# Optimization experiments

Measured on AMD Instinct MI355X. Metric: run time of the kernel, lower is better.

The kernel has to match this reference:

```python
import jax, jax.numpy as jnp
import numpy as np

HEADS = 16
PHI = (1.0 + np.sqrt(5.0)) / 2.0


def setup_inputs() -> dict:
    key = jax.random.key(0)
    k1, k2, k3, k4 = jax.random.split(key, 4)
    B, L, D = 2, 2048, 1024
    x = jax.random.normal(k1, (B, L, D), dtype=jnp.float32)
    # nn.Linear(dim, 3*dim, bias=False): store as [D, 3D] for x @ W
    w_qkv = jax.random.normal(k2, (D, 3 * D), dtype=jnp.float32) * (D ** -0.5)
    w_proj = jax.random.normal(k3, (D, D), dtype=jnp.float32) * (D ** -0.5)
    b_proj = jax.random.normal(k4, (D,), dtype=jnp.float32) * 0.01
    return {"x": x, "w_qkv": w_qkv, "w_proj": w_proj, "b_proj": b_proj}


def phi_bias(L):
    # pos[i] = (i * phi) mod 1 ; bias = log(exp(-|pos_i - pos_j|) + 1e-8)
    pos = (jnp.arange(L, dtype=jnp.float32) * PHI) % 1.0
    dist = jnp.abs(pos[:, None] - pos[None, :])  # [L, L]
    return jnp.log(jnp.exp(-dist) + 1e-8)


def reference(x, w_qkv, w_proj, b_proj):
    B, L, D = x.shape
    H = HEADS
    Dh = D // H
    scale = Dh ** -0.5
    qkv = (x @ w_qkv).reshape(B, L, 3, H, Dh)
    q = jnp.transpose(qkv[:, :, 0], (0, 2, 1, 3))  # [B, H, L, Dh]
    k = jnp.transpose(qkv[:, :, 1], (0, 2, 1, 3))
    v = jnp.transpose(qkv[:, :, 2], (0, 2, 1, 3))
    attn = jnp.einsum("bhid,bhjd->bhij", q, k) * scale  # [B, H, L, L]
    attn = attn + phi_bias(L)[None, None]  # additive phi-distance bias
    attn = jax.nn.softmax(attn, axis=-1)
    out = jnp.einsum("bhij,bhjd->bhid", attn, v)  # [B, H, L, Dh]
    out = jnp.transpose(out, (0, 2, 1, 3)).reshape(B, L, D)
    return out @ w_proj + b_proj
```

## Files before the change

### kernel.cpp

```cpp
#include <hip/hip_runtime.h>
#include <math.h>


typedef _Float16 f16;
typedef _Float16 f16x4 __attribute__((ext_vector_type(4)));
typedef _Float16 f16x8 __attribute__((ext_vector_type(8)));
typedef float f32x4 __attribute__((ext_vector_type(4)));

#define MFMA32(a, b, c) __builtin_amdgcn_mfma_f32_16x16x32_f16(a, b, c, 0, 0, 0)

static constexpr int Bsz = 2, Lseq = 2048, Dm = 1024, H = 16, Dh = 64;
static constexpr int Mtot = Bsz * Lseq;
static constexpr int NQKV = 3 * Dm;
static constexpr float PHI_F = 1.61803398874989484820f;
static constexpr float LOG2E = 1.44269504088896f;
static constexpr float QS = 0.125f * LOG2E;
static constexpr float CSTEP = 0.55417527999932633f;

__device__ __forceinline__ void load16_to_lds(const f16* g, f16* l) {
  __builtin_amdgcn_global_load_lds(
      (const __attribute__((address_space(1))) unsigned int*)g,
      (__attribute__((address_space(3))) unsigned int*)l, 16, 0, 0);
}

__global__ __launch_bounds__(256) void cast_f32_f16(const float* __restrict__ in,
                                                    f16* __restrict__ out, int n) {
  int i = (blockIdx.x * 256 + threadIdx.x) * 4;
  if (i < n) {
    float4 v = *reinterpret_cast<const float4*>(in + i);
    f16 t[4] = {(f16)v.x, (f16)v.y, (f16)v.z, (f16)v.w};
    *reinterpret_cast<uint2*>(out + i) = *reinterpret_cast<uint2*>(t);
  }
}

__global__ __launch_bounds__(256) void transpose_cast(const float* __restrict__ in,
                                                      f16* __restrict__ out,
                                                      int K, int N) {
  __shared__ float tile[32][33];
  int n0 = blockIdx.x * 32, k0 = blockIdx.y * 32;
  int tx = threadIdx.x & 31, ty = threadIdx.x >> 5;
#pragma unroll
  for (int r = 0; r < 32; r += 8)
    tile[ty + r][tx] = in[(size_t)(k0 + ty + r) * N + n0 + tx];
  __syncthreads();
#pragma unroll
  for (int r = 0; r < 32; r += 8)
    out[(size_t)(n0 + ty + r) * K + k0 + tx] = (f16)tile[tx][ty + r];
}

__global__ __launch_bounds__(256) void v_transpose(const f16* __restrict__ in,
                                                   f16* __restrict__ out) {
  __shared__ f16 td[64][68];
  int bh = blockIdx.y, l0 = blockIdx.x * 64;
  int tid = threadIdx.x;
  const f16* src = in + (size_t)bh * Lseq * Dh;
#pragma unroll
  for (int c = tid; c < 512; c += 256) {
    int row = c >> 3, col = (c & 7) * 8;
    uint4 v = *reinterpret_cast<const uint4*>(src + (size_t)(l0 + row) * Dh + col);
    f16 tmp[8];
    *reinterpret_cast<uint4*>(tmp) = v;
#pragma unroll
    for (int j = 0; j < 8; j++) td[col + j][row] = tmp[j];
  }
  __syncthreads();
  f16* dst = out + (size_t)bh * Dh * Lseq;
#pragma unroll
  for (int c = tid; c < 512; c += 256) {
    int d = c >> 3, m = (c & 7) * 8;
    f16 tmp[8];
#pragma unroll
    for (int j = 0; j < 8; j++) tmp[j] = td[d][m + j];
    *reinterpret_cast<uint4*>(dst + (size_t)d * Lseq + l0 + m) =
        *reinterpret_cast<uint4*>(tmp);
  }
}

template <int MODE>
__global__ __launch_bounds__(256) void gemm_f16(
    const f16* __restrict__ A, const f16* __restrict__ Bt,
    int M, int N, int K,
    f16* __restrict__ qb, f16* __restrict__ kb, f16* __restrict__ vl,
    float* __restrict__ out, const float* __restrict__ bias) {
  constexpr int BM = (MODE == 0) ? 128 : 64;
  constexpr int MI = BM / 32;
  constexpr int AI = BM / 32;
  __shared__ f16 As[BM * 64];
  __shared__ f16 Bs[128 * 64];

  int tid = threadIdx.x;
  int wave = tid >> 6, lane = tid & 63;
  int quad = lane >> 4, l16 = lane & 15;
  int wm = (wave >> 1) * (MI * 16), wn = (wave & 1) * 64;

  int lid = blockIdx.x;
  int xcd = lid & 7, t = lid >> 3;
  int m0, n0;
  if (MODE == 0) {
    int mg = xcd >> 1, ng = xcd & 1;
    m0 = (mg * 8 + t / 12) * 128;
    n0 = (ng * 12 + t % 12) * 128;
  } else {
    m0 = (xcd * 8 + (t >> 3)) * 64;
    n0 = (t & 7) * 128;
  }

  const int gu = (lane & 7) ^ ((lane >> 3) & 7);
  const f16* gA[AI];
  f16* lA[AI];
#pragma unroll
  for (int i = 0; i < AI; i++) {
    int it = wave * AI + i;
    gA[i] = A + (size_t)(m0 + it * 8 + (lane >> 3)) * K + gu * 8;
    lA[i] = As + it * 512;
  }
  const f16* gB[4];
  f16* lB[4];
#pragma unroll
  for (int i = 0; i < 4; i++) {
    int it = wave * 4 + i;
    gB[i] = Bt + (size_t)(n0 + it * 8 + (lane >> 3)) * K + gu * 8;
    lB[i] = Bs + it * 512;
  }

  f32x4 acc[MI][4] = {};

  for (int k0 = 0; k0 < K; k0 += 64) {
#pragma unroll
    for (int i = 0; i < AI; i++) load16_to_lds(gA[i] + k0, lA[i]);
#pragma unroll
    for (int i = 0; i < 4; i++) load16_to_lds(gB[i] + k0, lB[i]);
    __syncthreads();
#pragma unroll
    for (int s = 0; s < 2; s++) {
      f16x8 a[MI], b[4];
#pragma unroll
      for (int i = 0; i < MI; i++) {
        int row = wm + i * 16 + l16;
        a[i] = *reinterpret_cast<const f16x8*>(
            As + row * 64 + (((s * 4 + quad) ^ (l16 & 7)) * 8));
      }
#pragma unroll
      for (int j = 0; j < 4; j++) {
        int row = wn + j * 16 + l16;
        b[j] = *reinterpret_cast<const f16x8*>(
            Bs + row * 64 + (((s * 4 + quad) ^ (l16 & 7)) * 8));
      }
#pragma unroll
      for (int i = 0; i < MI; i++)
#pragma unroll
        for (int j = 0; j < 4; j++)
          acc[i][j] = MFMA32(a[i], b[j], acc[i][j]);
    }
    __syncthreads();
  }

#pragma unroll
  for (int i = 0; i < MI; i++) {
#pragma unroll
    for (int j = 0; j < 4; j++) {
      int n = n0 + wn + j * 16 + l16;
#pragma unroll
      for (int r = 0; r < 4; r++) {
        int m = m0 + wm + i * 16 + quad * 4 + r;
        if (MODE == 0) {
          int ty = n >> 10;
          int df = n & 1023;
          int h = df >> 6, dh = df & 63;
          int b = m >> 11, l = m & 2047;
          size_t idx = (((size_t)(b * H + h)) * Lseq + l) * Dh + dh;
          if (ty == 0)
            qb[idx] = (f16)(acc[i][j][r] * QS);
          else if (ty == 1)
            kb[idx] = (f16)acc[i][j][r];
          else
            vl[idx] = (f16)acc[i][j][r];
        } else {
          out[(size_t)m * N + n] = acc[i][j][r] + bias[n];
        }
      }
    }
  }
}

__global__ __launch_bounds__(256, 4) void attn_kernel(
    const f16* __restrict__ qb,
    const f16* __restrict__ kb,
    const f16* __restrict__ vb,
    f16* __restrict__ ctx) {
  __shared__ __align__(16) unsigned char smem[17408];
  f16* Ks = (f16*)smem;
  f16* Vs = (f16*)(smem + 9216);

  int bh = blockIdx.y;
  int q0 = blockIdx.x * 64;
  int tid = threadIdx.x, wave = tid >> 6, lane = tid & 63;
  int quad = lane >> 4, l16 = lane & 15;
  int jhalf = wave >> 1, qhalf = wave & 1;

  f16x8 qfrag[2][2];
  float pq[2];
#pragma unroll
  for (int set = 0; set < 2; set++) {
    int q = q0 + qhalf * 32 + set * 16 + l16;
    const f16* Qrow = qb + ((size_t)bh * Lseq + q) * Dh;
    qfrag[set][0] = *reinterpret_cast<const f16x8*>(Qrow + quad * 8);
    qfrag[set][1] = *reinterpret_cast<const f16x8*>(Qrow + 32 + quad * 8);
    pq[set] = fmodf((float)q * PHI_F, 1.0f);
  }

  float pk[2][4];
#pragma unroll
  for (int jb = 0; jb < 2; jb++)
#pragma unroll
    for (int r = 0; r < 4; r++) {
      int j = jhalf * 32 + jb * 16 + quad * 4 + r;
      pk[jb][r] = fmodf((float)j * PHI_F, 1.0f);
    }

  int uoff0 = ((jhalf * 4 + 0 + (quad >> 1)) ^ (l16 & 7)) * 8 + (quad & 1) * 4;
  int uoff1 = ((jhalf * 4 + 2 + (quad >> 1)) ^ (l16 & 7)) * 8 + (quad & 1) * 4;

  const f16 one = (f16)1.0f;
  const f16x8 ones8 = {one, one, one, one, one, one, one, one};

  f32x4 acc_o[2][4] = {};
  f32x4 acc_l[2] = {};

  const f16* Kbh = kb + (size_t)bh * Lseq * Dh;
  const f16* Vbh = vb + (size_t)bh * Dh * Lseq;

  for (int j0 = 0; j0 < Lseq; j0 += 64) {
    __syncthreads();
#pragma unroll
    for (int c = tid; c < 512; c += 256) {
      int row = c >> 3, col = (c & 7) * 8;
      *reinterpret_cast<uint4*>(Ks + row * 72 + col) =
          *reinterpret_cast<const uint4*>(Kbh + (size_t)(j0 + row) * Dh + col);
    }
#pragma unroll
    for (int c = tid; c < 512; c += 256) {
      int row = c >> 3, u = c & 7;
      int us = u ^ (row & 7);
      *reinterpret_cast<uint4*>(Vs + row * 64 + us * 8) =
          *reinterpret_cast<const uint4*>(Vbh + (size_t)row * Lseq + j0 + u * 8);
    }
    __syncthreads();

    f32x4 accs[2][2] = {};
#pragma unroll
    for (int s = 0; s < 2; s++)
#pragma unroll
      for (int jb = 0; jb < 2; jb++) {
        f16x8 kf = *reinterpret_cast<const f16x8*>(
            Ks + (jhalf * 32 + jb * 16 + l16) * 72 + s * 32 + quad * 8);
        accs[0][jb] = MFMA32(kf, qfrag[0][s], accs[0][jb]);
        accs[1][jb] = MFMA32(kf, qfrag[1][s], accs[1][jb]);
      }

    f16x8 pf8[2];
#pragma unroll
    for (int set = 0; set < 2; set++) {
#pragma unroll
      for (int jb = 0; jb < 2; jb++) {
        float p[4];
#pragma unroll
        for (int r = 0; r < 4; r++) {
          float d = pq[set] - pk[jb][r];
          float arg = fmaf(-LOG2E, fabsf(d), accs[set][jb][r]);
          p[r] = __builtin_amdgcn_exp2f(arg);
        }
        auto lo = __builtin_amdgcn_cvt_pkrtz(p[0], p[1]);
        auto hi = __builtin_amdgcn_cvt_pkrtz(p[2], p[3]);
        pf8[set][jb * 4 + 0] = lo[0];
        pf8[set][jb * 4 + 1] = lo[1];
        pf8[set][jb * 4 + 2] = hi[0];
        pf8[set][jb * 4 + 3] = hi[1];
      }
      acc_l[set] = MFMA32(ones8, pf8[set], acc_l[set]);
    }
#pragma unroll
    for (int jb = 0; jb < 2; jb++)
#pragma unroll
      for (int r = 0; r < 4; r++) {
        float tt = pk[jb][r] + CSTEP;
        pk[jb][r] = tt - floorf(tt);
      }

#pragma unroll
    for (int dblk = 0; dblk < 4; dblk++) {
      const f16* vrow = Vs + (dblk * 16 + l16) * 64;
      f16x4 v0 = *reinterpret_cast<const f16x4*>(vrow + uoff0);
      f16x4 v1 = *reinterpret_cast<const f16x4*>(vrow + uoff1);
      f16x8 va;
      va[0] = v0[0]; va[1] = v0[1]; va[2] = v0[2]; va[3] = v0[3];
      va[4] = v1[0]; va[5] = v1[1]; va[6] = v1[2]; va[7] = v1[3];
      acc_o[0][dblk] = MFMA32(va, pf8[0], acc_o[0][dblk]);
      acc_o[1][dblk] = MFMA32(va, pf8[1], acc_o[1][dblk]);
    }
  }

  __syncthreads();
  float* Oex = (float*)smem;
  float* Lex = (float*)(smem + 16384);
  if (jhalf == 1) {
#pragma unroll
    for (int set = 0; set < 2; set++) {
#pragma unroll
      for (int dblk = 0; dblk < 4; dblk++)
#pragma unroll
        for (int r = 0; r < 4; r++)
          Oex[(((qhalf * 2 + set) * 4 + dblk) * 16 + quad * 4 + r) * 16 + l16] =
              acc_o[set][dblk][r];
      if (quad == 0) Lex[(qhalf * 2 + set) * 16 + l16] = acc_l[set][0];
    }
  }
  __syncthreads();
  if (jhalf == 0) {
    int b = bh >> 4, h = bh & 15;
#pragma unroll
    for (int set = 0; set < 2; set++) {
      float ltot = acc_l[set][0] + Lex[(qhalf * 2 + set) * 16 + l16];
      float inv = 1.0f / ltot;
      int q = q0 + qhalf * 32 + set * 16 + l16;
      f16* crow = ctx + (size_t)(b * Lseq + q) * Dm + h * 64;
#pragma unroll
      for (int dblk = 0; dblk < 4; dblk++) {
        f16x4 o;
#pragma unroll
        for (int r = 0; r < 4; r++) {
          float full = acc_o[set][dblk][r] +
              Oex[(((qhalf * 2 + set) * 4 + dblk) * 16 + quad * 4 + r) * 16 + l16];
          o[r] = (f16)(full * inv);
        }
        *reinterpret_cast<uint2*>(crow + dblk * 16 + quad * 4) =
            *reinterpret_cast<uint2*>(&o);
      }
    }
  }
}

extern "C" void kernel_launch(void* const* d_in, const int* in_sizes, int n_in,
                              void* d_out, int out_size, void* d_ws, size_t ws_size,
                              hipStream_t stream) {
  const float* x      = (const float*)d_in[0];
  const float* w_qkv  = (const float*)d_in[1];
  const float* w_proj = (const float*)d_in[2];
  const float* b_proj = (const float*)d_in[3];
  float* out = (float*)d_out;

  f16* xb    = (f16*)d_ws;
  f16* wqkvT = xb + (size_t)Mtot * Dm;
  f16* wpT   = wqkvT + (size_t)NQKV * Dm;
  f16* qb    = wpT + (size_t)Dm * Dm;
  f16* kb    = qb + (size_t)Bsz * H * Lseq * Dh;
  f16* vb    = kb + (size_t)Bsz * H * Lseq * Dh;
  f16* ctx   = vb + (size_t)Bsz * H * Lseq * Dh;
  f16* vl    = ctx;

  cast_f32_f16<<<(Mtot * Dm) / (256 * 4), 256, 0, stream>>>(x, xb, Mtot * Dm);
  transpose_cast<<<dim3(NQKV / 32, Dm / 32), 256, 0, stream>>>(w_qkv, wqkvT, Dm, NQKV);
  transpose_cast<<<dim3(Dm / 32, Dm / 32), 256, 0, stream>>>(w_proj, wpT, Dm, Dm);

  gemm_f16<0><<<768, 256, 0, stream>>>(
      xb, wqkvT, Mtot, NQKV, Dm, qb, kb, vl, nullptr, nullptr);

  v_transpose<<<dim3(Lseq / 64, Bsz * H), 256, 0, stream>>>(vl, vb);

  attn_kernel<<<dim3(Lseq / 64, Bsz * H), 256, 0, stream>>>(qb, kb, vb, ctx);

  gemm_f16<1><<<512, 256, 0, stream>>>(
      ctx, wpT, Mtot, Dm, Dm, nullptr, nullptr, nullptr, out, b_proj);
}
```

Measured before the change: 205.0 us.

## Use direct global-to-LDS loads for K/V tiles and pre-permute V layout

Measured after the change: 192.5 us. -6.1%, faster.

```diff
diff --git a/kernel.cpp b/kernel.cpp
--- a/kernel.cpp
+++ b/kernel.cpp
@@ -67,11 +67,14 @@
   f16* dst = out + (size_t)bh * Dh * Lseq;
 #pragma unroll
   for (int c = tid; c < 512; c += 256) {
-    int d = c >> 3, m = (c & 7) * 8;
+    int d = c >> 3, co = c & 7;
+    int jh = co >> 2, qd = co & 3;
     f16 tmp[8];
 #pragma unroll
-    for (int j = 0; j < 8; j++) tmp[j] = td[d][m + j];
-    *reinterpret_cast<uint4*>(dst + (size_t)d * Lseq + l0 + m) =
+    for (int e = 0; e < 4; e++) tmp[e] = td[d][jh * 32 + qd * 4 + e];
+#pragma unroll
+    for (int e = 0; e < 4; e++) tmp[4 + e] = td[d][jh * 32 + 16 + qd * 4 + e];
+    *reinterpret_cast<uint4*>(dst + (size_t)d * Lseq + l0 + co * 8) =
         *reinterpret_cast<uint4*>(tmp);
   }
 }
@@ -105,7 +108,7 @@
     n0 = (t & 7) * 128;
   }
 
-  const int gu = (lane & 7) ^ ((lane >> 3) & 7);
+  const int gu = (lane & 7) ^ (lane >> 3);
   const f16* gA[AI];
   f16* lA[AI];
 #pragma unroll
@@ -188,9 +191,9 @@
     const f16* __restrict__ kb,
     const f16* __restrict__ vb,
     f16* __restrict__ ctx) {
-  __shared__ __align__(16) unsigned char smem[17408];
+  __shared__ __align__(16) unsigned char smem[16640];
   f16* Ks = (f16*)smem;
-  f16* Vs = (f16*)(smem + 9216);
+  f16* Vs = (f16*)(smem + 8192);
 
   int bh = blockIdx.y;
   int q0 = blockIdx.x * 64;
@@ -218,8 +221,21 @@
       pk[jb][r] = fmodf((float)j * PHI_F, 1.0f);
     }
 
-  int uoff0 = ((jhalf * 4 + 0 + (quad >> 1)) ^ (l16 & 7)) * 8 + (quad & 1) * 4;
-  int uoff1 = ((jhalf * 4 + 2 + (quad >> 1)) ^ (l16 & 7)) * 8 + (quad & 1) * 4;
+  const f16* Kbh = kb + (size_t)bh * Lseq * Dh;
+  const f16* Vbh = vb + (size_t)bh * Dh * Lseq;
+  const int gu = (lane & 7) ^ (lane >> 3);
+  const f16* gK[2];
+  const f16* gV[2];
+  f16* lK[2];
+  f16* lV[2];
+#pragma unroll
+  for (int i = 0; i < 2; i++) {
+    int g8 = (wave * 2 + i) * 8 + (lane >> 3);
+    gK[i] = Kbh + (size_t)g8 * Dh + gu * 8;
+    gV[i] = Vbh + (size_t)g8 * Lseq + gu * 8;
+    lK[i] = Ks + (wave * 2 + i) * 512;
+    lV[i] = Vs + (wave * 2 + i) * 512;
+  }
 
   const f16 one = (f16)1.0f;
   const f16x8 ones8 = {one, one, one, one, one, one, one, one};
@@ -227,23 +243,12 @@
   f32x4 acc_o[2][4] = {};
   f32x4 acc_l[2] = {};
 
-  const f16* Kbh = kb + (size_t)bh * Lseq * Dh;
-  const f16* Vbh = vb + (size_t)bh * Dh * Lseq;
-
   for (int j0 = 0; j0 < Lseq; j0 += 64) {
     __syncthreads();
 #pragma unroll
-    for (int c = tid; c < 512; c += 256) {
-      int row = c >> 3, col = (c & 7) * 8;
-      *reinterpret_cast<uint4*>(Ks + row * 72 + col) =
-          *reinterpret_cast<const uint4*>(Kbh + (size_t)(j0 + row) * Dh + col);
-    }
-#pragma unroll
-    for (int c = tid; c < 512; c += 256) {
-      int row = c >> 3, u = c & 7;
-      int us = u ^ (row & 7);
-      *reinterpret_cast<uint4*>(Vs + row * 64 + us * 8) =
-          *reinterpret_cast<const uint4*>(Vbh + (size_t)row * Lseq + j0 + u * 8);
+    for (int i = 0; i < 2; i++) {
+      load16_to_lds(gK[i] + (size_t)j0 * Dh, lK[i]);
+      load16_to_lds(gV[i] + j0, lV[i]);
     }
     __syncthreads();
 
@@ -253,7 +258,7 @@
 #pragma unroll
       for (int jb = 0; jb < 2; jb++) {
         f16x8 kf = *reinterpret_cast<const f16x8*>(
-            Ks + (jhalf * 32 + jb * 16 + l16) * 72 + s * 32 + quad * 8);
+            Ks + (jhalf * 32 + jb * 16 + l16) * 64 + (((s * 4 + quad) ^ (l16 & 7)) * 8));
         accs[0][jb] = MFMA32(kf, qfrag[0][s], accs[0][jb]);
         accs[1][jb] = MFMA32(kf, qfrag[1][s], accs[1][jb]);
       }
@@ -282,19 +287,14 @@
 #pragma unroll
     for (int jb = 0; jb < 2; jb++)
 #pragma unroll
-      for (int r = 0; r < 4; r++) {
-        float tt = pk[jb][r] + CSTEP;
-        pk[jb][r] = tt - floorf(tt);
-      }
+      for (int r = 0; r < 4; r++)
+        pk[jb][r] = __builtin_amdgcn_fractf(pk[jb][r] + CSTEP);
 
 #pragma unroll
     for (int dblk = 0; dblk < 4; dblk++) {
-      const f16* vrow = Vs + (dblk * 16 + l16) * 64;
-      f16x4 v0 = *reinterpret_cast<const f16x4*>(vrow + uoff0);
-      f16x4 v1 = *reinterpret_cast<const f16x4*>(vrow + uoff1);
-      f16x8 va;
-      va[0] = v0[0]; va[1] = v0[1]; va[2] = v0[2]; va[3] = v0[3];
-      va[4] = v1[0]; va[5] = v1[1]; va[6] = v1[2]; va[7] = v1[3];
+      int row = dblk * 16 + l16;
+      f16x8 va = *reinterpret_cast<const f16x8*>(
+          Vs + row * 64 + (((jhalf * 4 + quad) ^ (l16 & 7)) * 8));
       acc_o[0][dblk] = MFMA32(va, pf8[0], acc_o[0][dblk]);
       acc_o[1][dblk] = MFMA32(va, pf8[1], acc_o[1][dblk]);
     }
```
